# Kernel optimization log

Measured on AMD Instinct MI355X. Metric: run time of the kernel, lower is better.

Reference implementation:

```python
import jax, jax.numpy as jnp
from jax import lax
import numpy as np

A = 9            # anchors per location (3 scales x 3 ratios)
STRIDE = 16      # feat_stride
PRE_NMS = 6000   # top-k proposals before NMS (test mode)
POST_NMS = 300   # proposals kept after NMS (test mode)
NMS_T = 0.7      # NMS IoU threshold
MIN_SIZE = 16.0  # min proposal side length


def _anchor_ref(base=16, ratios=(0.5, 1.0, 2.0), scales=(8, 16, 32)):
    """Standard py-faster-rcnn anchor references, shape (9, 4)."""
    ratios = np.array(ratios, np.float64)
    scales = np.array(scales, np.float64)
    ctr = (base - 1) / 2.0
    size = float(base * base)
    ws = np.round(np.sqrt(size / ratios))
    hs = np.round(ws * ratios)
    ra = np.stack([ctr - 0.5 * (ws - 1), ctr - 0.5 * (hs - 1),
                   ctr + 0.5 * (ws - 1), ctr + 0.5 * (hs - 1)], 1)
    out = []
    for a in ra:
        w = a[2] - a[0] + 1.0
        h = a[3] - a[1] + 1.0
        cx = a[0] + 0.5 * (w - 1)
        cy = a[1] + 0.5 * (h - 1)
        ws2 = w * scales
        hs2 = h * scales
        out.append(np.stack([cx - 0.5 * (ws2 - 1), cy - 0.5 * (hs2 - 1),
                             cx + 0.5 * (ws2 - 1), cy + 0.5 * (hs2 - 1)], 1))
    return jnp.asarray(np.concatenate(out, 0), jnp.float32)


def _nms_keep(boxes):
    """Greedy NMS on score-sorted boxes (N,4) -> bool keep mask (N,)."""
    x1, y1, x2, y2 = boxes[:, 0], boxes[:, 1], boxes[:, 2], boxes[:, 3]
    areas = (x2 - x1 + 1.0) * (y2 - y1 + 1.0)
    iw = jnp.clip(jnp.minimum(x2[:, None], x2[None, :]) - jnp.maximum(x1[:, None], x1[None, :]) + 1.0, 0.0)
    ih = jnp.clip(jnp.minimum(y2[:, None], y2[None, :]) - jnp.maximum(y1[:, None], y1[None, :]) + 1.0, 0.0)
    inter = iw * ih
    iou = inter / (areas[:, None] + areas[None, :] - inter)
    n = boxes.shape[0]
    idx = jnp.arange(n)
    def body(i, keep):
        sup = (iou[i] > NMS_T) & (idx > i)
        return jnp.where(keep[i], keep & ~sup, keep)
    return lax.fori_loop(0, n, body, jnp.ones((n,), bool))


def _rpn_forward(feature_map, W_rpn, b_rpn, W_score, b_score, W_bbox, b_bbox, img_size):
    dn = ('NHWC', 'HWIO', 'NHWC')
    rpn = lax.conv_general_dilated(feature_map, W_rpn, (1, 1), 'SAME', dimension_numbers=dn) + b_rpn
    rpn = jax.nn.relu(rpn)
    cls = lax.conv_general_dilated(rpn, W_score, (1, 1), 'SAME', dimension_numbers=dn) + b_score
    bbx = lax.conv_general_dilated(rpn, W_bbox, (1, 1), 'SAME', dimension_numbers=dn) + b_bbox
    n, h, w, _ = feature_map.shape
    cls = cls.reshape(n, h, w, A, 2)
    prob = jax.nn.softmax(cls, axis=-1)
    fg = prob[..., 1].reshape(-1)           # (h*w*A,) foreground prob
    deltas = bbx.reshape(-1, 4)             # (h*w*A, 4)
    # anchors: shifts over (h, w), anchor-ref inner -> matches (h,w,A) flattening
    ref = _anchor_ref()
    sx = jnp.arange(w, dtype=jnp.float32) * STRIDE
    sy = jnp.arange(h, dtype=jnp.float32) * STRIDE
    ys, xs = jnp.meshgrid(sy, sx, indexing='ij')
    shifts = jnp.stack([xs, ys, xs, ys], -1).reshape(-1, 1, 4)
    anchors = (shifts + ref[None]).reshape(-1, 4)
    # decode deltas -> boxes
    aw = anchors[:, 2] - anchors[:, 0] + 1.0
    ah = anchors[:, 3] - anchors[:, 1] + 1.0
    acx = anchors[:, 0] + 0.5 * aw
    acy = anchors[:, 1] + 0.5 * ah
    pcx = deltas[:, 0] * aw + acx
    pcy = deltas[:, 1] * ah + acy
    pw = jnp.exp(deltas[:, 2]) * aw
    ph = jnp.exp(deltas[:, 3]) * ah
    imh = img_size[0].astype(jnp.float32)
    imw = img_size[1].astype(jnp.float32)
    boxes = jnp.stack([
        jnp.clip(pcx - 0.5 * pw, 0.0, imw - 1.0),
        jnp.clip(pcy - 0.5 * ph, 0.0, imh - 1.0),
        jnp.clip(pcx + 0.5 * pw, 0.0, imw - 1.0),
        jnp.clip(pcy + 0.5 * ph, 0.0, imh - 1.0)], -1)
    # min-size filter
    bw = boxes[:, 2] - boxes[:, 0] + 1.0
    bh = boxes[:, 3] - boxes[:, 1] + 1.0
    fg = jnp.where((bw >= MIN_SIZE) & (bh >= MIN_SIZE), fg, -1e9)
    # pre-NMS top-k (sorted descending)
    top_s, top_i = lax.top_k(fg, PRE_NMS)
    top_b = boxes[top_i]
    keep = _nms_keep(lax.stop_gradient(top_b))
    sel_s = jnp.where(keep, top_s, -1e9)
    _, sel_i = lax.top_k(sel_s, POST_NMS)
    rois = top_b[sel_i]
    ok = keep[sel_i] & (sel_s[sel_i] > -1e8)
    return jnp.where(ok[:, None], rois, 0.0)  # (POST_NMS, 4), zero-padded


def setup_inputs() -> dict:
    key = jax.random.key(0)
    ks = jax.random.split(key, 7)
    C_in, C_mid = 1024, 512
    std = 0.01
    return {
        'feature_map': jax.random.normal(ks[0], (1, 100, 150, C_in), jnp.float32),
        'W_rpn': jax.random.normal(ks[1], (3, 3, C_in, C_mid), jnp.float32) * std,
        'b_rpn': jnp.zeros((C_mid,), jnp.float32),
        'W_score': jax.random.normal(ks[2], (1, 1, C_mid, A * 2), jnp.float32) * std,
        'b_score': jnp.zeros((A * 2,), jnp.float32),
        'W_bbox': jax.random.normal(ks[3], (1, 1, C_mid, A * 4), jnp.float32) * std,
        'b_bbox': jnp.zeros((A * 4,), jnp.float32),
        'img_size': jnp.array([1600, 2400], jnp.int32),
    }


def reference(feature_map, W_rpn, b_rpn, W_score, b_score, W_bbox, b_bbox, img_size):
    return _rpn_forward(feature_map, W_rpn, b_rpn, W_score, b_score, W_bbox, b_bbox, img_size)
```

## Files before the change

### kernel.cpp

```cpp
#include <hip/hip_runtime.h>
#include <hip/hip_bf16.h>

typedef unsigned int u32;
typedef unsigned long long u64;

#define H_FM 100
#define W_FM 150
#define CIN 1024
#define CMID 512
#define NPIX 15000
#define NANCH 135000
#define PRE_NMS_N 6000
#define POST_NMS_N 300
#define WPR 94

typedef __attribute__((ext_vector_type(8))) short short8;
typedef __attribute__((ext_vector_type(8))) __bf16 bf16x8;
typedef __attribute__((ext_vector_type(4))) float f32x4;

__device__ __forceinline__ u32 fkey(float f) {
  u32 u = __float_as_uint(f);
  return (u & 0x80000000u) ? ~u : (u | 0x80000000u);
}

__device__ __forceinline__ u64 shfl64(u64 v, int src) {
  u32 lo = (u32)__shfl((int)(u32)v, src, 64);
  u32 hi = (u32)__shfl((int)(u32)(v >> 32), src, 64);
  return ((u64)hi << 32) | (u64)lo;
}

struct FragArg {
  short8 v;
  __device__ operator short8() const { return v; }
  __device__ operator bf16x8() const { return __builtin_bit_cast(bf16x8, v); }
};
__device__ __forceinline__ f32x4 mfma16(short8 a, short8 b, f32x4 c) {
  return __builtin_amdgcn_mfma_f32_16x16x32_bf16(FragArg{a}, FragArg{b}, c, 0, 0, 0);
}

#define GLL(gp, lp) __builtin_amdgcn_global_load_lds(                        \
    (const __attribute__((address_space(1))) unsigned int*)(gp),             \
    (__attribute__((address_space(3))) unsigned int*)(lp), 16, 0, 0)

__device__ __forceinline__ void split3(float f, unsigned short& a,
                                       unsigned short& b, unsigned short& c) {
  __hip_bfloat16 h0 = __float2bfloat16(f);
  float f0 = __bfloat162float(h0);
  float r1 = f - f0;
  __hip_bfloat16 h1 = __float2bfloat16(r1);
  float r2 = r1 - __bfloat162float(h1);
  __hip_bfloat16 h2 = __float2bfloat16(r2);
  a = *(unsigned short*)&h0;
  b = *(unsigned short*)&h1;
  c = *(unsigned short*)&h2;
}

__global__ __launch_bounds__(256) void k_split_fm(
    const float* __restrict__ src, unsigned short* __restrict__ d0,
    unsigned short* __restrict__ d1, unsigned short* __restrict__ d2,
    float* __restrict__ zp)
{
  if (blockIdx.x == 0 && threadIdx.x < 64) zp[threadIdx.x] = 0.f;
  const int n4 = NPIX * CIN / 4;
  for (int i = blockIdx.x * 256 + threadIdx.x; i < n4; i += gridDim.x * 256) {
    float4 v = ((const float4*)src)[i];
    float f[4] = {v.x, v.y, v.z, v.w};
    ushort4 o0, o1, o2;
    unsigned short* p0 = (unsigned short*)&o0;
    unsigned short* p1 = (unsigned short*)&o1;
    unsigned short* p2 = (unsigned short*)&o2;
    #pragma unroll
    for (int e = 0; e < 4; ++e) split3(f[e], p0[e], p1[e], p2[e]);
    ((ushort4*)d0)[i] = o0;
    ((ushort4*)d1)[i] = o1;
    ((ushort4*)d2)[i] = o2;
  }
}

__global__ __launch_bounds__(256) void k_split_wt(
    const float* __restrict__ Wsrc, unsigned short* __restrict__ t0,
    unsigned short* __restrict__ t1, unsigned short* __restrict__ t2)
{
  __shared__ float tile[64][65];
  const int k0 = blockIdx.x * 64;
  const int n0 = blockIdx.y * 64;
  const int tid = threadIdx.x;
  const int lr = tid >> 4;
  const int lc = (tid & 15) * 4;
  #pragma unroll
  for (int rr = 0; rr < 64; rr += 16) {
    float4 v = *(const float4*)&Wsrc[(size_t)(k0 + lr + rr) * CMID + n0 + lc];
    tile[lr + rr][lc + 0] = v.x; tile[lr + rr][lc + 1] = v.y;
    tile[lr + rr][lc + 2] = v.z; tile[lr + rr][lc + 3] = v.w;
  }
  __syncthreads();
  const int n = tid >> 2;
  const int kk = (tid & 3) * 16;
  unsigned short b0[16], b1[16], b2[16];
  #pragma unroll
  for (int e = 0; e < 16; ++e) split3(tile[kk + e][n], b0[e], b1[e], b2[e]);
  size_t ob = ((size_t)(n0 + n) * 9216 + k0 + kk) >> 2;
  #pragma unroll
  for (int q = 0; q < 4; ++q) {
    ((ushort4*)t0)[ob + q] = *(ushort4*)&b0[q * 4];
    ((ushort4*)t1)[ob + q] = *(ushort4*)&b1[q * 4];
    ((ushort4*)t2)[ob + q] = *(ushort4*)&b2[q * 4];
  }
}

__global__ __launch_bounds__(256, 2) void k_conv5(
    const unsigned short* __restrict__ fm0, const unsigned short* __restrict__ fm1,
    const unsigned short* __restrict__ fm2, const unsigned short* __restrict__ wt0,
    const unsigned short* __restrict__ wt1, const unsigned short* __restrict__ wt2,
    const float* __restrict__ br, const float* __restrict__ zp,
    float* __restrict__ rpn)
{
  __shared__ char lds[61440];
  const int tid = threadIdx.x;
  const int lane = tid & 63;
  const int w = tid >> 6;
  const int bn = (blockIdx.x & 3) * 128;
  const int t = blockIdx.x >> 2;
  const int ty = t / 6, tx = t - ty * 6;
  const int py0 = ty * 5, px0 = tx * 25;
  const int wm = (w >> 1) * 64, wn = (w & 1) * 64;

  const unsigned short* fmP[3] = {fm0, fm1, fm2};
  const unsigned short* wtP[3] = {wt0, wt1, wt2};

  u64 asrc[9]; u32 amsk[9]; u32 adst[9];
  #pragma unroll
  for (int q = 0; q < 9; ++q) {
    int j36 = w * 9 + q;
    int s = j36 / 12, gg = j36 % 12;
    int c = gg / 3, part = gg - c * 3;
    int pix = part * 64 + lane;
    int uy = pix / 27, ux = pix - uy * 27;
    int gy = py0 + uy - 1, gx = px0 + ux - 1;
    bool valid = (pix < 189) && ((unsigned)gy < H_FM) && ((unsigned)gx < W_FM);
    asrc[q] = valid ? ((u64)(const char*)fmP[s] + (u64)(gy * W_FM + gx) * 2048 + c * 16)
                    : (u64)(const char*)zp;
    amsk[q] = valid ? 0xFFFFFFFFu : 0u;
    adst[q] = s * 12288 + c * 3072 + part * 1024;
  }
  u64 bsrc[6]; u32 bdst[6];
  #pragma unroll
  for (int q = 0; q < 6; ++q) {
    int j24 = w * 6 + q;
    int s = j24 >> 3, gg = j24 & 7;
    int c = gg >> 1, part = gg & 1;
    int row = part * 64 + lane;
    bsrc[q] = (u64)(const char*)wtP[s] + (u64)(bn + row) * 18432 + c * 16;
    bdst[q] = 36864u + s * 8192 + c * 2048 + part * 1024;
  }
  int abase[4];
  #pragma unroll
  for (int i = 0; i < 4; ++i) {
    int m = wm + i * 16 + (lane & 15);
    int y = m / 25, x = m - y * 25;
    abase[i] = y * 27 + x + 28;
  }
  const int aquad = (lane >> 4) * 3072;
  u32 boff[3][4];
  #pragma unroll
  for (int s = 0; s < 3; ++s)
    #pragma unroll
    for (int j = 0; j < 4; ++j)
      boff[s][j] = 36864u + s * 8192 + (lane >> 4) * 2048 + (wn + j * 16 + (lane & 15)) * 16;

  f32x4 acc[4][4];
  #pragma unroll
  for (int i = 0; i < 4; ++i)
    #pragma unroll
    for (int j = 0; j < 4; ++j) acc[i][j] = (f32x4){0.f, 0.f, 0.f, 0.f};

  for (int chb = 0; chb < 2048; chb += 64) {
    __syncthreads();
    #pragma unroll
    for (int q = 0; q < 9; ++q)
      GLL((const char*)(asrc[q] + (u64)(chb & amsk[q])), lds + adst[q]);
    for (int seg = 0; seg < 9; ++seg) {
      if (seg) __syncthreads();
      const u32 so = (u32)(seg * 2048 + chb);
      #pragma unroll
      for (int q = 0; q < 6; ++q)
        GLL((const char*)(bsrc[q] + so), lds + bdst[q]);
      __syncthreads();

      const int d = ((seg / 3) - 1) * 27 + (seg - (seg / 3) * 3 - 1);
      short8 B[3][4];
      #pragma unroll
      for (int s = 0; s < 3; ++s)
        #pragma unroll
        for (int j = 0; j < 4; ++j)
          B[s][j] = *(const short8*)(lds + boff[s][j]);
      #pragma unroll
      for (int i = 0; i < 4; ++i) {
        const int ap = (abase[i] + d) * 16 + aquad;
        short8 A0 = *(const short8*)(lds + ap);
        short8 A1 = *(const short8*)(lds + 12288 + ap);
        short8 A2 = *(const short8*)(lds + 24576 + ap);
        #pragma unroll
        for (int j = 0; j < 4; ++j) {
          f32x4 c = acc[i][j];
          c = mfma16(A0, B[0][j], c);
          c = mfma16(A0, B[1][j], c);
          c = mfma16(A1, B[0][j], c);
          c = mfma16(A1, B[1][j], c);
          c = mfma16(A0, B[2][j], c);
          c = mfma16(A2, B[0][j], c);
          acc[i][j] = c;
        }
      }
    }
  }

  #pragma unroll
  for (int i = 0; i < 4; ++i) {
    const int mb = wm + i * 16 + ((lane >> 4) << 2);
    #pragma unroll
    for (int r = 0; r < 4; ++r) {
      const int m = mb + r;
      if (m < 125) {
        int y = m / 25, x = m - y * 25;
        size_t gp = (size_t)((py0 + y) * W_FM + (px0 + x)) * CMID;
        #pragma unroll
        for (int j = 0; j < 4; ++j) {
          const int n = bn + wn + j * 16 + (lane & 15);
          rpn[gp + n] = fmaxf(acc[i][j][r] + br[n], 0.f);
        }
      }
    }
  }
}

__global__ __launch_bounds__(256) void k_packW(
    const float* __restrict__ Ws, const float* __restrict__ bs,
    const float* __restrict__ Wb, const float* __restrict__ bb,
    float* __restrict__ Wp, float* __restrict__ bp)
{
  int tt = blockIdx.x * 256 + threadIdx.x;
  int k = tt >> 6, o = tt & 63;
  float v = (o < 18) ? Ws[k * 18 + o] : ((o < 54) ? Wb[k * 36 + (o - 18)] : 0.f);
  Wp[tt] = v;
  if (tt < 64) bp[tt] = (tt < 18) ? bs[tt] : ((tt < 54) ? bb[tt - 18] : 0.f);
}

__global__ __launch_bounds__(256) void k_headgemm(
    const float* __restrict__ rpn, const float* __restrict__ Wp,
    const float* __restrict__ bp, float* __restrict__ vals)
{
  __shared__ float As[32][132];
  __shared__ float Bs[32][64];
  const int tid = threadIdx.x;
  const int bm = blockIdx.x * 128;
  const int mt = tid >> 3;
  const int nt = tid & 7;
  const int kg = tid & 7;
  const int ar = tid >> 3;
  const int n4 = (tid & 15) * 4;
  const int kr = tid >> 4;
  const float4 z4 = make_float4(0.f, 0.f, 0.f, 0.f);

  float acc[4][8];
  #pragma unroll
  for (int i = 0; i < 4; ++i)
    #pragma unroll
    for (int j = 0; j < 8; ++j) acc[i][j] = 0.f;

  for (int kc = 0; kc < 512; kc += 32) {
    __syncthreads();
    #pragma unroll
    for (int rr = 0; rr < 128; rr += 32) {
      int m = bm + ar + rr;
      float4 v = (m < NPIX) ? *(const float4*)&rpn[(size_t)m * CMID + kc + kg * 4] : z4;
      As[kg * 4 + 0][ar + rr] = v.x; As[kg * 4 + 1][ar + rr] = v.y;
      As[kg * 4 + 2][ar + rr] = v.z; As[kg * 4 + 3][ar + rr] = v.w;
    }
    *(float4*)&Bs[kr][n4]      = *(const float4*)&Wp[(kc + kr) * 64 + n4];
    *(float4*)&Bs[kr + 16][n4] = *(const float4*)&Wp[(kc + kr + 16) * 64 + n4];
    __syncthreads();
    #pragma unroll
    for (int kk = 0; kk < 32; ++kk) {
      float4 a = *(const float4*)&As[kk][mt * 4];
      float4 b0 = *(const float4*)&Bs[kk][nt * 8];
      float4 b1 = *(const float4*)&Bs[kk][nt * 8 + 4];
      float av[4] = {a.x, a.y, a.z, a.w};
      float bv[8] = {b0.x, b0.y, b0.z, b0.w, b1.x, b1.y, b1.z, b1.w};
      #pragma unroll
      for (int i = 0; i < 4; ++i)
        #pragma unroll
        for (int j = 0; j < 8; ++j) acc[i][j] = fmaf(av[i], bv[j], acc[i][j]);
    }
  }
  float bias[8];
  #pragma unroll
  for (int j = 0; j < 8; ++j) bias[j] = bp[nt * 8 + j];
  #pragma unroll
  for (int r = 0; r < 4; ++r) {
    int m = bm + mt * 4 + r;
    if (m < NPIX) {
      float o[8];
      #pragma unroll
      for (int j = 0; j < 8; ++j) o[j] = acc[r][j] + bias[j];
      float* op = vals + (size_t)m * 64 + nt * 8;
      *(float4*)op = *(float4*)&o[0];
      *(float4*)(op + 4) = *(float4*)&o[4];
    }
  }
}

__global__ __launch_bounds__(256) void k_decode(
    const float* __restrict__ vals, const int* __restrict__ img,
    float* __restrict__ fg, float4* __restrict__ boxes)
{
  int gi = blockIdx.x * 256 + threadIdx.x;
  if (gi >= NANCH) return;
  const int p = gi / 9, a = gi - p * 9;
  const float AW[9] = {184.f, 368.f, 736.f, 128.f, 256.f, 512.f,  88.f, 176.f, 352.f};
  const float AH[9] = { 96.f, 192.f, 384.f, 128.f, 256.f, 512.f, 176.f, 352.f, 704.f};
  const int y = p / W_FM, x = p - y * W_FM;
  const float* row = vals + (size_t)p * 64;

  float c0 = row[2 * a], c1 = row[2 * a + 1];
  float score = 1.f / (1.f + expf(c0 - c1));

  float dxv = row[18 + 4 * a + 0];
  float dyv = row[18 + 4 * a + 1];
  float dwv = row[18 + 4 * a + 2];
  float dhv = row[18 + 4 * a + 3];

  float aw = AW[a], ah = AH[a];
  float acx = (float)(x * 16 + 8);
  float acy = (float)(y * 16 + 8);
  float pcx = dxv * aw + acx;
  float pcy = dyv * ah + acy;
  float pw = expf(dwv) * aw;
  float ph = expf(dhv) * ah;

  float imh1 = (float)img[0] - 1.f;
  float imw1 = (float)img[1] - 1.f;
  float b0 = fminf(fmaxf(pcx - 0.5f * pw, 0.f), imw1);
  float b1 = fminf(fmaxf(pcy - 0.5f * ph, 0.f), imh1);
  float b2 = fminf(fmaxf(pcx + 0.5f * pw, 0.f), imw1);
  float b3 = fminf(fmaxf(pcy + 0.5f * ph, 0.f), imh1);

  float bw = b2 - b0 + 1.f, bh = b3 - b1 + 1.f;
  if (!(bw >= 16.f && bh >= 16.f)) score = -1e9f;

  fg[gi] = score;
  boxes[gi] = make_float4(b0, b1, b2, b3);
}

__global__ void k_init(u32* __restrict__ hist, u32* __restrict__ ctl) {
  hist[threadIdx.x] = 0;
  if (threadIdx.x == 0) { ctl[0] = 0; ctl[1] = PRE_NMS_N; ctl[2] = 0; ctl[3] = 0; }
}

__global__ __launch_bounds__(256) void k_hist(
    const float* __restrict__ fg, u32* __restrict__ hist,
    const u32* __restrict__ ctl, int pass)
{
  __shared__ u32 h[256];
  h[threadIdx.x] = 0;
  __syncthreads();
  const int shift = 24 - 8 * pass;
  const u32 prefix = ctl[0];
  for (int i = blockIdx.x * 256 + threadIdx.x; i < NANCH; i += 128 * 256) {
    u32 key = fkey(fg[i]);
    bool match = (pass == 0) || ((key >> (shift + 8)) == prefix);
    if (match) atomicAdd(&h[(key >> shift) & 255], 1u);
  }
  __syncthreads();
  u32 c = h[threadIdx.x];
  if (c) atomicAdd(&hist[threadIdx.x], c);
}

__global__ void k_scan(u32* __restrict__ hist, u32* __restrict__ ctl) {
  if (threadIdx.x == 0) {
    u32 kneed = ctl[1];
    u32 cum = 0;
    int d = 0;
    for (int dd = 255; dd >= 0; --dd) {
      u32 c = hist[dd];
      if (cum + c >= kneed) { d = dd; break; }
      cum += c;
    }
    ctl[0] = (ctl[0] << 8) | (u32)d;
    ctl[1] = kneed - cum;
  }
  __syncthreads();
  hist[threadIdx.x] = 0;
}

__global__ __launch_bounds__(256) void k_compact(
    const float* __restrict__ fg, u32* __restrict__ ctl,
    u64* __restrict__ listA, u32* __restrict__ listB)
{
  int i = blockIdx.x * 256 + threadIdx.x;
  if (i >= NANCH) return;
  u32 T = ctl[0];
  u32 key = fkey(fg[i]);
  if (key > T) {
    u32 slot = atomicAdd(&ctl[2], 1u);
    listA[slot] = ((u64)key << 32) | (u64)(0xFFFFFFFFu - (u32)i);
  } else if (key == T) {
    u32 slot = atomicAdd(&ctl[3], 1u);
    if (slot < 8192) listB[slot] = (u32)i;
  }
}

__global__ __launch_bounds__(256) void k_tiefix(
    u32* __restrict__ ctl, const u32* __restrict__ listB, u64* __restrict__ listA)
{
  __shared__ u32 s[8192];
  const int tid = threadIdx.x;
  const u32 kneed = ctl[1];
  const u32 base = ctl[2];
  const u32 cntB = min(ctl[3], 8192u);
  const u32 T = ctl[0];
  if (kneed == 0) return;
  if (cntB == kneed) {
    for (u32 t = tid; t < kneed; t += 256)
      listA[base + t] = ((u64)T << 32) | (u64)(0xFFFFFFFFu - listB[t]);
    return;
  }
  u32 n2 = 1;
  while (n2 < cntB) n2 <<= 1;
  for (u32 i = tid; i < n2; i += 256) s[i] = (i < cntB) ? listB[i] : 0xFFFFFFFFu;
  __syncthreads();
  for (u32 k = 2; k <= n2; k <<= 1) {
    for (u32 j = k >> 1; j > 0; j >>= 1) {
      for (u32 i = tid; i < n2; i += 256) {
        u32 ixj = i ^ j;
        if (ixj > i) {
          u32 a = s[i], b = s[ixj];
          bool up = ((i & k) == 0);
          if ((a > b) == up) { s[i] = b; s[ixj] = a; }
        }
      }
      __syncthreads();
    }
  }
  for (u32 t = tid; t < kneed; t += 256)
    listA[base + t] = ((u64)T << 32) | (u64)(0xFFFFFFFFu - s[t]);
}

__global__ __launch_bounds__(1024) void k_sort(
    const u64* __restrict__ listA, u64* __restrict__ sorted)
{
  __shared__ u64 s[8192];
  const int tid = threadIdx.x;
  for (int i = tid; i < 8192; i += 1024) s[i] = (i < PRE_NMS_N) ? listA[i] : 0ull;
  __syncthreads();
  for (int k = 2; k <= 8192; k <<= 1) {
    for (int j = k >> 1; j > 0; j >>= 1) {
      for (int i = tid; i < 8192; i += 1024) {
        int ixj = i ^ j;
        if (ixj > i) {
          u64 a = s[i], b = s[ixj];
          bool up = ((i & k) == 0);
          if ((a < b) == up) { s[i] = b; s[ixj] = a; }
        }
      }
      __syncthreads();
    }
  }
  for (int i = tid; i < 8192; i += 1024) sorted[i] = s[i];
}

__global__ __launch_bounds__(256) void k_gather(
    const u64* __restrict__ sorted, const float4* __restrict__ boxes,
    float4* __restrict__ tb)
{
  int t = blockIdx.x * 256 + threadIdx.x;
  if (t >= PRE_NMS_N) return;
  u64 p = sorted[t];
  u32 idx = 0xFFFFFFFFu - (u32)(p & 0xFFFFFFFFull);
  tb[t] = boxes[idx];
}

__global__ __launch_bounds__(64) void k_mask(
    const float4* __restrict__ tb, u64* __restrict__ mask)
{
  __shared__ float4 cb[64];
  const int bj = blockIdx.x, bi = blockIdx.y, t = threadIdx.x;
  const int j0 = bj * 64;
  const int jn = min(64, PRE_NMS_N - j0);
  if (t < jn) cb[t] = tb[j0 + t];
  __syncthreads();
  const int i = bi * 64 + t;
  if (i >= PRE_NMS_N) return;
  const float4 b = tb[i];
  const float ai = (b.z - b.x + 1.f) * (b.w - b.y + 1.f);
  u64 bits = 0;
  for (int tt = 0; tt < jn; ++tt) {
    int j = j0 + tt;
    if (j <= i) continue;
    float4 c = cb[tt];
    float iw = fminf(b.z, c.z) - fmaxf(b.x, c.x) + 1.f;
    float ih = fminf(b.w, c.w) - fmaxf(b.y, c.y) + 1.f;
    float inter = fmaxf(iw, 0.f) * fmaxf(ih, 0.f);
    float aj = (c.z - c.x + 1.f) * (c.w - c.y + 1.f);
    float iou = inter / (ai + aj - inter);
    if (iou > 0.7f) bits |= (1ull << tt);
  }
  mask[(size_t)i * WPR + bj] = bits;
}

__global__ __launch_bounds__(64) void k_nms(
    const u64* __restrict__ mask, const float* __restrict__ tb,
    const u64* __restrict__ sorted, float* __restrict__ out)
{
  const int lane = threadIdx.x;
  u64 r0 = 0, r1 = 0;
  int kept = 0;
  const u32 kcut = fkey(-1e8f);
  for (int i = 0; i < PRE_NMS_N; ++i) {
    const int w = i >> 6, b = i & 63;
    u64 v0 = shfl64(r0, w & 63);
    u64 v1 = shfl64(r1, w & 63);
    u64 word = (w < 64) ? v0 : v1;
    if (!((word >> b) & 1ull)) {
      u32 key = (u32)(sorted[i] >> 32);
      if (key <= kcut) break;
      if (lane < 4) out[kept * 4 + lane] = tb[i * 4 + lane];
      ++kept;
      if (kept >= POST_NMS_N) break;
      const u64* row = mask + (size_t)i * WPR;
      r0 |= row[lane];
      if (lane < WPR - 64) r1 |= row[64 + lane];
    }
  }
  for (int j = kept * 4 + lane; j < POST_NMS_N * 4; j += 64) out[j] = 0.f;
}

extern "C" void kernel_launch(void* const* d_in, const int* in_sizes, int n_in,
                              void* d_out, int out_size, void* d_ws, size_t ws_size,
                              hipStream_t stream) {
  const float* fm  = (const float*)d_in[0];
  const float* Wr  = (const float*)d_in[1];
  const float* br  = (const float*)d_in[2];
  const float* Wsc = (const float*)d_in[3];
  const float* bsc = (const float*)d_in[4];
  const float* Wbb = (const float*)d_in[5];
  const float* bbb = (const float*)d_in[6];
  const int*   img = (const int*)d_in[7];
  float* out = (float*)d_out;

  char* w = (char*)d_ws;
  size_t off = 0;
  auto alloc = [&](size_t bytes) {
    size_t p = off;
    off = (off + bytes + 255) & ~(size_t)255;
    return p;
  };
  float* rpn    = (float*)(w + alloc((size_t)NPIX * CMID * 4));
  float* fg     = (float*)(w + alloc((size_t)NANCH * 4));
  float4* boxes = (float4*)(w + alloc((size_t)NANCH * 16));
  u32* hist     = (u32*)(w + alloc(1024));
  u32* ctl      = (u32*)(w + alloc(64));
  u64* listA    = (u64*)(w + alloc((size_t)PRE_NMS_N * 8));
  u32* listB    = (u32*)(w + alloc(8192 * 4));
  u64* sorted   = (u64*)(w + alloc(8192 * 8));
  float4* topbox= (float4*)(w + alloc((size_t)PRE_NMS_N * 16));
  u64* mask     = (u64*)(w + alloc((size_t)PRE_NMS_N * WPR * 8));
  float* zp     = (float*)(w + alloc(256));
  float* Wp     = (float*)(w + alloc(512 * 64 * 4));
  float* bp     = (float*)(w + alloc(64 * 4));
  float* vals   = (float*)(w + alloc((size_t)NPIX * 64 * 4));
  size_t fb = (size_t)NPIX * CIN * 2;
  size_t wb = (size_t)9216 * CMID * 2;
  unsigned short* fm0 = (unsigned short*)(w + alloc(fb));
  unsigned short* fm1 = (unsigned short*)(w + alloc(fb));
  unsigned short* fm2 = (unsigned short*)(w + alloc(fb));
  unsigned short* wt0 = (unsigned short*)(w + alloc(wb));
  unsigned short* wt1 = (unsigned short*)(w + alloc(wb));
  unsigned short* wt2 = (unsigned short*)(w + alloc(wb));

  k_split_fm<<<dim3(1024), dim3(256), 0, stream>>>(fm, fm0, fm1, fm2, zp);
  k_split_wt<<<dim3(144, 8), dim3(256), 0, stream>>>(Wr, wt0, wt1, wt2);
  k_packW<<<dim3(128), dim3(256), 0, stream>>>(Wsc, bsc, Wbb, bbb, Wp, bp);
  k_conv5<<<dim3(120 * 4), dim3(256), 0, stream>>>(
      fm0, fm1, fm2, wt0, wt1, wt2, br, zp, rpn);
  k_headgemm<<<dim3(118), dim3(256), 0, stream>>>(rpn, Wp, bp, vals);
  k_decode<<<dim3((NANCH + 255) / 256), dim3(256), 0, stream>>>(vals, img, fg, boxes);
  k_init<<<1, 256, 0, stream>>>(hist, ctl);
  for (int pass = 0; pass < 4; ++pass) {
    k_hist<<<128, 256, 0, stream>>>(fg, hist, ctl, pass);
    k_scan<<<1, 256, 0, stream>>>(hist, ctl);
  }
  k_compact<<<(NANCH + 255) / 256, 256, 0, stream>>>(fg, ctl, listA, listB);
  k_tiefix<<<1, 256, 0, stream>>>(ctl, listB, listA);
  k_sort<<<1, 1024, 0, stream>>>(listA, sorted);
  k_gather<<<(PRE_NMS_N + 255) / 256, 256, 0, stream>>>(sorted, boxes, topbox);
  k_mask<<<dim3(WPR, WPR), 64, 0, stream>>>(topbox, mask);
  k_nms<<<1, 64, 0, stream>>>(mask, (const float*)topbox, sorted, out);
}
```

Baseline: 1.408 ms.

## Restructure conv GEMM into flat-pixel 128x64 tiles with swizzled double-staged LDS

Replaces the spatial-halo conv tile (5x25 pixels, 128 output channels, shared A halo reused across 9 taps) with a flat implicit-GEMM tile of 128 pixels by 64 channels. Each of the 288 k-steps gathers A per tap directly from global memory, and the next tile's load is issued before the current MFMAs run. LDS shrinks, an XOR swizzle is added, and occupancy rises to 3 blocks per CU across 944 blocks. The trade is that feature-map halo reuse is lost, so more A traffic goes to global/L2 memory, and each block computes a smaller N tile.

After: 1.943 ms. +38.0%, slower.

```diff
diff --git a/kernel.cpp b/kernel.cpp
--- a/kernel.cpp
+++ b/kernel.cpp
@@ -108,126 +108,128 @@
   }
 }
 
-__global__ __launch_bounds__(256, 2) void k_conv5(
+__global__ __launch_bounds__(256, 3) void k_conv7(
     const unsigned short* __restrict__ fm0, const unsigned short* __restrict__ fm1,
     const unsigned short* __restrict__ fm2, const unsigned short* __restrict__ wt0,
     const unsigned short* __restrict__ wt1, const unsigned short* __restrict__ wt2,
     const float* __restrict__ br, const float* __restrict__ zp,
     float* __restrict__ rpn)
 {
-  __shared__ char lds[61440];
+  __shared__ char lds[36864];
   const int tid = threadIdx.x;
-  const int lane = tid & 63;
+  const int ll = tid & 63;
   const int w = tid >> 6;
-  const int bn = (blockIdx.x & 3) * 128;
-  const int t = blockIdx.x >> 2;
-  const int ty = t / 6, tx = t - ty * 6;
-  const int py0 = ty * 5, px0 = tx * 25;
-  const int wm = (w >> 1) * 64, wn = (w & 1) * 64;
-
-  const unsigned short* fmP[3] = {fm0, fm1, fm2};
-  const unsigned short* wtP[3] = {wt0, wt1, wt2};
-
-  u64 asrc[9]; u32 amsk[9]; u32 adst[9];
-  #pragma unroll
-  for (int q = 0; q < 9; ++q) {
-    int j36 = w * 9 + q;
-    int s = j36 / 12, gg = j36 % 12;
-    int c = gg / 3, part = gg - c * 3;
-    int pix = part * 64 + lane;
-    int uy = pix / 27, ux = pix - uy * 27;
-    int gy = py0 + uy - 1, gx = px0 + ux - 1;
-    bool valid = (pix < 189) && ((unsigned)gy < H_FM) && ((unsigned)gx < W_FM);
-    asrc[q] = valid ? ((u64)(const char*)fmP[s] + (u64)(gy * W_FM + gx) * 2048 + c * 16)
-                    : (u64)(const char*)zp;
-    amsk[q] = valid ? 0xFFFFFFFFu : 0u;
-    adst[q] = s * 12288 + c * 3072 + part * 1024;
-  }
-  u64 bsrc[6]; u32 bdst[6];
-  #pragma unroll
-  for (int q = 0; q < 6; ++q) {
-    int j24 = w * 6 + q;
-    int s = j24 >> 3, gg = j24 & 7;
-    int c = gg >> 1, part = gg & 1;
-    int row = part * 64 + lane;
-    bsrc[q] = (u64)(const char*)wtP[s] + (u64)(bn + row) * 18432 + c * 16;
-    bdst[q] = 36864u + s * 8192 + c * 2048 + part * 1024;
-  }
-  int abase[4];
+  const int bn = (blockIdx.x & 7) * 64;
+  const int bm = (blockIdx.x >> 3) * 128;
+  const int wm = (w >> 1) * 64;
+  const int wn = (w & 1) * 32;
+
+  const int lp = ll >> 2;
+  const u32 sqb = (u32)((ll & 3) ^ ((ll >> 3) & 3)) * 16u;
+
+  const int pm0 = bm + w * 16 + lp;
+  const int pm1 = bm + (w + 4) * 16 + lp;
+  const int y0 = pm0 / W_FM, x0 = pm0 - y0 * W_FM;
+  const int y1 = pm1 / W_FM, x1 = pm1 - y1 * W_FM;
+  const bool mv0 = pm0 < NPIX, mv1 = pm1 < NPIX;
+
+  const u32 boff = (u32)(bn + w * 16 + lp) * 18432u + sqb;
+
+  const int fr = ll & 15;
+  const u32 fswzb = (u32)((ll >> 4) ^ ((fr >> 1) & 3)) * 16u;
+  const u32 aAddr = (u32)(wm + fr) * 64u + fswzb;
+  const u32 bAddr = 24576u + (u32)(wn + fr) * 64u + fswzb;
+
+  const char* fmB[3] = {(const char*)fm0, (const char*)fm1, (const char*)fm2};
+  const char* wtB[3] = {(const char*)wt0, (const char*)wt1, (const char*)wt2};
+  const char* zpb = (const char*)zp + sqb;
+
+  u32 aofs0 = 0, aofs1 = 0;
+  bool av0 = false, av1 = false;
+
+  auto segSetup = [&](int seg) {
+    int dy = seg / 3 - 1, dx = seg - (seg / 3) * 3 - 1;
+    int sy0 = y0 + dy, sx0 = x0 + dx;
+    int sy1 = y1 + dy, sx1 = x1 + dx;
+    av0 = mv0 && (unsigned)sy0 < H_FM && (unsigned)sx0 < W_FM;
+    av1 = mv1 && (unsigned)sy1 < H_FM && (unsigned)sx1 < W_FM;
+    aofs0 = (u32)(sy0 * W_FM + sx0) * 2048u + sqb;
+    aofs1 = (u32)(sy1 * W_FM + sx1) * 2048u + sqb;
+  };
+
+  auto stage = [&](int seg, u32 chb) {
+    #pragma unroll
+    for (int s = 0; s < 3; ++s) {
+      const char* g0 = av0 ? (fmB[s] + aofs0 + chb) : zpb;
+      const char* g1 = av1 ? (fmB[s] + aofs1 + chb) : zpb;
+      GLL(g0, lds + s * 8192 + w * 1024);
+      GLL(g1, lds + s * 8192 + (w + 4) * 1024);
+    }
+    const u32 ko = (u32)seg * 2048u + chb;
+    #pragma unroll
+    for (int s = 0; s < 3; ++s)
+      GLL(wtB[s] + (boff + ko), lds + 24576 + s * 4096 + w * 1024);
+  };
+
+  short8 Af[3][4], Bf[3][2];
+  auto readFrags = [&]() {
+    #pragma unroll
+    for (int s = 0; s < 3; ++s) {
+      #pragma unroll
+      for (int i = 0; i < 4; ++i)
+        Af[s][i] = *(const short8*)(lds + aAddr + s * 8192 + i * 1024);
+      #pragma unroll
+      for (int j = 0; j < 2; ++j)
+        Bf[s][j] = *(const short8*)(lds + bAddr + s * 4096 + j * 1024);
+    }
+  };
+
+  f32x4 acc[4][2];
+  #pragma unroll
+  for (int i = 0; i < 4; ++i)
+    #pragma unroll
+    for (int j = 0; j < 2; ++j) acc[i][j] = (f32x4){0.f, 0.f, 0.f, 0.f};
+
+  segSetup(0);
+  stage(0, 0);
+  __syncthreads();
+  readFrags();
+
+  for (int it = 0; it < 288; ++it) {
+    const int nit = it + 1;
+    const bool more = nit < 288;
+    if (more && (nit & 31) == 0) segSetup(nit >> 5);
+    __syncthreads();
+    if (more) stage(nit >> 5, (u32)(nit & 31) * 64u);
+    #pragma unroll
+    for (int i = 0; i < 4; ++i)
+      #pragma unroll
+      for (int j = 0; j < 2; ++j) {
+        f32x4 c = acc[i][j];
+        c = mfma16(Af[0][i], Bf[0][j], c);
+        c = mfma16(Af[0][i], Bf[1][j], c);
+        c = mfma16(Af[1][i], Bf[0][j], c);
+        c = mfma16(Af[1][i], Bf[1][j], c);
+        c = mfma16(Af[0][i], Bf[2][j], c);
+        c = mfma16(Af[2][i], Bf[0][j], c);
+        acc[i][j] = c;
+      }
+    __syncthreads();
+    if (more) readFrags();
+  }
+
   #pragma unroll
   for (int i = 0; i < 4; ++i) {
-    int m = wm + i * 16 + (lane & 15);
-    int y = m / 25, x = m - y * 25;
-    abase[i] = y * 27 + x + 28;
-  }
-  const int aquad = (lane >> 4) * 3072;
-  u32 boff[3][4];
-  #pragma unroll
-  for (int s = 0; s < 3; ++s)
-    #pragma unroll
-    for (int j = 0; j < 4; ++j)
-      boff[s][j] = 36864u + s * 8192 + (lane >> 4) * 2048 + (wn + j * 16 + (lane & 15)) * 16;
-
-  f32x4 acc[4][4];
-  #pragma unroll
-  for (int i = 0; i < 4; ++i)
-    #pragma unroll
-    for (int j = 0; j < 4; ++j) acc[i][j] = (f32x4){0.f, 0.f, 0.f, 0.f};
-
-  for (int chb = 0; chb < 2048; chb += 64) {
-    __syncthreads();
-    #pragma unroll
-    for (int q = 0; q < 9; ++q)
-      GLL((const char*)(asrc[q] + (u64)(chb & amsk[q])), lds + adst[q]);
-    for (int seg = 0; seg < 9; ++seg) {
-      if (seg) __syncthreads();
-      const u32 so = (u32)(seg * 2048 + chb);
-      #pragma unroll
-      for (int q = 0; q < 6; ++q)
-        GLL((const char*)(bsrc[q] + so), lds + bdst[q]);
-      __syncthreads();
-
-      const int d = ((seg / 3) - 1) * 27 + (seg - (seg / 3) * 3 - 1);
-      short8 B[3][4];
-      #pragma unroll
-      for (int s = 0; s < 3; ++s)
-        #pragma unroll
-        for (int j = 0; j < 4; ++j)
-          B[s][j] = *(const short8*)(lds + boff[s][j]);
-      #pragma unroll
-      for (int i = 0; i < 4; ++i) {
-        const int ap = (abase[i] + d) * 16 + aquad;
-        short8 A0 = *(const short8*)(lds + ap);
-        short8 A1 = *(const short8*)(lds + 12288 + ap);
-        short8 A2 = *(const short8*)(lds + 24576 + ap);
-        #pragma unroll
-        for (int j = 0; j < 4; ++j) {
-          f32x4 c = acc[i][j];
-          c = mfma16(A0, B[0][j], c);
-          c = mfma16(A0, B[1][j], c);
-          c = mfma16(A1, B[0][j], c);
-          c = mfma16(A1, B[1][j], c);
-          c = mfma16(A0, B[2][j], c);
-          c = mfma16(A2, B[0][j], c);
-          acc[i][j] = c;
-        }
-      }
-    }
-  }
-
-  #pragma unroll
-  for (int i = 0; i < 4; ++i) {
-    const int mb = wm + i * 16 + ((lane >> 4) << 2);
+    const int mb = bm + wm + i * 16 + ((ll >> 4) << 2);
     #pragma unroll
     for (int r = 0; r < 4; ++r) {
       const int m = mb + r;
-      if (m < 125) {
-        int y = m / 25, x = m - y * 25;
-        size_t gp = (size_t)((py0 + y) * W_FM + (px0 + x)) * CMID;
+      if (m < NPIX) {
+        float* op = rpn + (size_t)m * CMID;
         #pragma unroll
-        for (int j = 0; j < 4; ++j) {
-          const int n = bn + wn + j * 16 + (lane & 15);
-          rpn[gp + n] = fmaxf(acc[i][j][r] + br[n], 0.f);
+        for (int j = 0; j < 2; ++j) {
+          const int n = bn + wn + j * 16 + (ll & 15);
+          op[n] = fmaxf(acc[i][j][r] + br[n], 0.f);
         }
       }
     }
@@ -581,7 +583,7 @@
   k_split_fm<<<dim3(1024), dim3(256), 0, stream>>>(fm, fm0, fm1, fm2, zp);
   k_split_wt<<<dim3(144, 8), dim3(256), 0, stream>>>(Wr, wt0, wt1, wt2);
   k_packW<<<dim3(128), dim3(256), 0, stream>>>(Wsc, bsc, Wbb, bbb, Wp, bp);
-  k_conv5<<<dim3(120 * 4), dim3(256), 0, stream>>>(
+  k_conv7<<<dim3(118 * 8), dim3(256), 0, stream>>>(
       fm0, fm1, fm2, wt0, wt1, wt2, br, zp, rpn);
   k_headgemm<<<dim3(118), dim3(256), 0, stream>>>(rpn, Wp, bp, vals);
   k_decode<<<dim3((NANCH + 255) / 256), dim3(256), 0, stream>>>(vals, img, fg, boxes);
```
